# Kernel tuning notes

Hardware: AMD Instinct MI355X
Metric: run time of the kernel (lower is better)

## Reference

```python
import jax, jax.numpy as jnp
import numpy as np

L = 11
THETA_DIV = 5
OMEGA0 = 6
BLUR_K = 7
BLUR_SIGMA = 4.0


def _make_psi(j_scale):
    # Morlet wavelet bank exactly as np.fromfunction in the torch module
    c = L // 2
    k = np.arange(THETA_DIV, dtype=np.float64)[:, None, None]
    i = np.arange(L, dtype=np.float64)[None, :, None]
    jj = np.arange(L, dtype=np.float64)[None, None, :]
    scale = 2.0 * 2.0 ** (2 * j_scale)
    arg = (1j * OMEGA0 * ((i - c) * np.cos(np.pi * k / THETA_DIV)
                          - (jj - c) * np.sin(np.pi * k / THETA_DIV)) / scale
           - ((i - c) ** 2 + (jj - c) ** 2) / scale)
    return (1.0 / (np.sqrt(2.0 * np.pi) * 2.0 ** j_scale)) * np.exp(arg)


def _make_blur_kernel():
    # 7x7 Gaussian, sigma=4, normalized to sum 1 (standard GaussianBlur)
    c = (BLUR_K - 1) / 2.0
    x = np.arange(BLUR_K, dtype=np.float64) - c
    g = np.exp(-(x ** 2) / (2.0 * BLUR_SIGMA ** 2))
    k2 = np.outer(g, g)
    return (k2 / k2.sum()).astype(np.float32)


def setup_inputs() -> dict:
    key = jax.random.key(0)
    img = jax.random.normal(key, (8, 1, 256, 256), dtype=jnp.float32)
    psi = np.concatenate([_make_psi(3), _make_psi(0)], axis=0)  # [10,11,11] complex
    psi_re = jnp.asarray(psi.real.astype(np.float32)[:, None, :, :])  # [10,1,11,11]
    psi_im = jnp.asarray(psi.imag.astype(np.float32)[:, None, :, :])
    blur_k = jnp.asarray(_make_blur_kernel())  # [7,7]
    return {"img": img, "psi_re": psi_re, "psi_im": psi_im, "blur_k": blur_k}


def _conv(x, w, groups=1, pad=5):
    return jax.lax.conv_general_dilated(
        x, w, window_strides=(1, 1), padding=[(pad, pad), (pad, pad)],
        dimension_numbers=("NCHW", "OIHW", "NCHW"), feature_group_count=groups)


def _blur(x, blur_k):
    # depthwise Gaussian blur, padding 'same'
    C = x.shape[1]
    w = jnp.tile(blur_k[None, None], (C, 1, 1, 1))  # [C,1,7,7]
    return _conv(x, w, groups=C, pad=BLUR_K // 2)


def reference(img, psi_re, psi_im, blur_k):
    # s0: blurred input, strided downsample by 8
    s0 = _blur(img, blur_k)[:, :, ::8, ::8]

    # s1 = conv2d(img_complex, psi1): img is real, so split into re/im real convs
    s1_re = _conv(img, psi_re)            # [N,10,H,W]
    s1_im = _conv(img, psi_im)
    s1_abs = jnp.sqrt(s1_re * s1_re + s1_im * s1_im)
    # blurred s1 is later cast to double -> only its real part survives;
    # blur is a real-linear op so Re(blur(s1)) = blur(Re(s1))
    s1_out = _blur(s1_re, blur_k)[:, :, ::8, ::8]

    # s2 = grouped conv of |s1| with psi2 (psi1 tiled over 10 groups)
    psi2_re = jnp.tile(psi_re, (10, 1, 1, 1))  # [100,1,11,11]
    # only real part of blur(s2) reaches the output (cast to double)
    s2_re = _conv(s1_abs, psi2_re, groups=10)  # [N,100,H,W]
    s2_out = _blur(s2_re, blur_k)[:, :, ::8, ::8]

    feature = jnp.concatenate([s0, s1_out, s2_out], axis=1)  # [N,111,H/8,W/8]
    N = feature.shape[0]
    return feature.reshape(N, -1)
```

## Files before the change

### kernel.cpp

```cpp
#include <hip/hip_runtime.h>
#include <math.h>


#define PIMG_SZ (288 * 288)
#define FHP_OFF (8 * PIMG_SZ)
#define SSTR  284
#define W1    298
#define S1SZ  (17 * 298)
#define IVSTR 300
#define IVPL  (17 * 300)
#define CSTR  600

__global__ __launch_bounds__(256) void k_prep(const float* __restrict__ img,
                                              const float* __restrict__ psi_re,
                                              const float* __restrict__ psi_im,
                                              const float* __restrict__ blur,
                                              float* __restrict__ pimg,
                                              float* __restrict__ fhp) {
    int bid = blockIdx.x, tid = threadIdx.x;
    if (bid < 288) {
        int n = bid / 36, rg = bid - n * 36;
        float* dst = pimg + n * PIMG_SZ + rg * 8 * 288;
        const float* src = img + n * 65536;
        for (int i = tid; i < 576; i += 256) {
            int lr = i / 72, c4 = i - lr * 72;
            int prow = rg * 8 + lr;
            int irow = prow - 16;
            float4 v = {0.f, 0.f, 0.f, 0.f};
            if (irow >= 0 && irow < 256 && c4 >= 4 && c4 < 68)
                v = *(const float4*)(src + irow * 256 + 4 * c4 - 16);
            *(float4*)(dst + lr * 288 + 4 * c4) = v;
        }
        return;
    }
    for (int g = tid; g < 1360; g += 256) {
        int ch = g / 136;
        int w = g - ch * 136;
        int part = w / 17;
        int i = w - part * 17;
        const float* pr = psi_re + ch * 121;
        const float* pi = psi_im + ch * 121;
        float val = 0.f;
        if (part < 4) {
            int qmin = (part >= 2) ? 3 : 0;
            int comp = part & 1;
            float bden = blur[24];
            for (int q = qmin; q < 7; ++q) {
                int jj = i - q;
                if (jj < 0 || jj > 10) continue;
                float bq = blur[21 + q] / bden;
                float hh = comp ? pi[55 + jj] : pr[55 + jj];
                val += bq * hh;
            }
        } else {
            int pmin = (part >= 6) ? 3 : 0;
            int comp = part & 1;
            float dr = pr[60], di = pi[60];
            float inv = 1.f / (dr * dr + di * di);
            for (int p = pmin; p < 7; ++p) {
                int ii = i - p;
                if (ii < 0 || ii > 10) continue;
                float ap = blur[p * 7 + 3];
                float nr = pr[ii * 11 + 5], ni = pi[ii * 11 + 5];
                float f = comp ? (ni * dr - nr * di) * inv
                               : (nr * dr + ni * di) * inv;
                val += ap * f;
            }
        }
        fhp[g] = val;
    }
}

__global__ __launch_bounds__(512, 4) void k_fused4(const float* __restrict__ pimg,
                                                   const float* __restrict__ psi_re,
                                                   const float* __restrict__ psi_im,
                                                   const float* __restrict__ blur,
                                                   const float* __restrict__ fhp,
                                                   float* __restrict__ out) {
    __shared__ __align__(16) float bufA[10132];
    __shared__ __align__(16) float bufB[10200];
    const int tid = threadIdx.x;
    const int lane = tid & 63;
    const int wave = tid >> 6;
    const int Y = blockIdx.x;
    const int src2 = blockIdx.y;
    const int n = blockIdx.z;
    size_t nb = (size_t)n * 111 * 1024;

    const bool isimg = (src2 == 0);
    const bool paired = (src2 >= 3);
    int ga = 0, gb = 0;
    if (src2 == 1) ga = gb = 0;
    else if (src2 == 2) ga = gb = 5;
    else if (paired) {
        int p2 = src2 - 3;
        ga = (p2 < 2) ? 1 + p2 : 4 + p2;
        gb = (p2 < 2) ? 4 - p2 : 11 - p2;
    }

    if (isimg) {
        const float* gp = pimg + n * PIMG_SZ + (8 * Y + 8) * 288 + 8;
        for (int idx = tid; idx < 17 * 68; idx += 512) {
            int r = idx / 68, c4 = idx - r * 68;
            float4 v = *(const float4*)(gp + r * 288 + 4 * c4);
            int c = 4 * c4;
            int d = r * W1 + c + (c >> 3);
            bufA[d] = v.x; bufA[d + 1] = v.y; bufA[d + 2] = v.z; bufA[d + 3] = v.w;
        }
    } else {
        const float* pr = psi_re + ga * 121;
        const float* pi = psi_im + ga * 121;
        float dr = pr[60], di = pi[60];
        float inv = rsqrtf(dr * dr + di * di);

        const float* gp = pimg + n * PIMG_SZ + (8 * Y + 3) * 288 + 8;
        for (int idx = tid; idx < 27 * 68; idx += 512) {
            int r = idx / 68, c4 = idx - r * 68;
            *(float4*)(bufA + r * SSTR + 4 * c4) = *(const float4*)(gp + r * 288 + 4 * c4);
        }
        __syncthreads();

        for (int task = tid; task < 532; task += 512) {
            int rg = (task >= 266) ? 1 : 0;
            int v = task - rg * 266;
            int r0 = rg * 8;
            const float* sp = bufA + r0 * SSTR + v + 3;
            float xv[18];
#pragma unroll
            for (int p = 0; p < 18; ++p) xv[p] = sp[p * SSTR];
            int dsw = v + (v >> 3);
            float* dR = bufB + r0 * IVSTR + dsw;
#pragma unroll
            for (int m = 0; m < 8; ++m) {
                float ar = 0.f, ai = 0.f;
#pragma unroll
                for (int p = 0; p < 11; ++p) {
                    ar = fmaf(pr[p * 11 + 5], xv[m + p], ar);
                    ai = fmaf(pi[p * 11 + 5], xv[m + p], ai);
                }
                dR[m * IVSTR] = ar;
                dR[m * IVSTR + IVPL] = ai;
            }
        }
        if (tid < 266) {
            int v = tid;
            const float* sp = bufA + 16 * SSTR + v + 3;
            float ar = 0.f, ai = 0.f;
#pragma unroll
            for (int p = 0; p < 11; ++p) {
                float x = sp[p * SSTR];
                ar = fmaf(pr[p * 11 + 5], x, ar);
                ai = fmaf(pi[p * 11 + 5], x, ai);
            }
            int dsw = v + (v >> 3);
            bufB[16 * IVSTR + dsw] = ar;
            bufB[16 * IVSTR + IVPL + dsw] = ai;
        }
        __syncthreads();

        int rowbase = 8 * Y - 8;
        for (int t2 = tid; t2 < 544; t2 += 512) {
            int r = t2 >> 5, xg = t2 & 31;
            int ry = rowbase + r;
            int wb = r * W1 + 9 * xg + 9;
            if (ry >= 0 && ry < 256) {
                const float* sR = bufB + r * IVSTR + 9 * xg;
                float xr[18], xi[18];
#pragma unroll
                for (int j = 0; j < 18; ++j) {
                    int off = j + (j >> 3);
                    xr[j] = sR[off];
                    xi[j] = sR[off + IVPL];
                }
                if (paired) {
#pragma unroll
                    for (int m = 0; m < 8; ++m) {
                        float a = 0.f, b = 0.f, c = 0.f, d = 0.f;
#pragma unroll
                        for (int j = 0; j < 11; ++j) {
                            float hr = pr[55 + j], hi2 = pi[55 + j];
                            a = fmaf(hr, xr[m + j], a);
                            b = fmaf(hi2, xi[m + j], b);
                            c = fmaf(hr, xi[m + j], c);
                            d = fmaf(hi2, xr[m + j], d);
                        }
                        float e1 = a - b, o1 = c + d;
                        float e2 = a + b, o2 = c - d;
                        bufA[wb + m]        = inv * sqrtf(fmaf(e1, e1, o1 * o1));
                        bufA[S1SZ + wb + m] = inv * sqrtf(fmaf(e2, e2, o2 * o2));
                    }
                } else {
#pragma unroll
                    for (int m = 0; m < 8; ++m) {
                        float sr = 0.f, si = 0.f;
#pragma unroll
                        for (int j = 0; j < 11; ++j) {
                            float hr = pr[55 + j], hi2 = pi[55 + j];
                            sr = fmaf(hr, xr[m + j], fmaf(-hi2, xi[m + j], sr));
                            si = fmaf(hr, xi[m + j], fmaf(hi2, xr[m + j], si));
                        }
                        bufA[wb + m] = inv * sqrtf(fmaf(sr, sr, si * si));
                    }
                }
            } else {
#pragma unroll
                for (int m = 0; m < 8; ++m) {
                    bufA[wb + m] = 0.f;
                    if (paired) bufA[S1SZ + wb + m] = 0.f;
                }
            }
        }
        if (tid < 17) {
            int r = tid;
#pragma unroll
            for (int t = 0; t < 8; ++t) {
                bufA[r * W1 + t] = 0.f;
                if (paired) bufA[S1SZ + r * W1 + t] = 0.f;
            }
            bufA[r * W1 + 297] = 0.f;
            if (paired) bufA[S1SZ + r * W1 + 297] = 0.f;
        }
    }
    __syncthreads();

    {
        int kh = __builtin_amdgcn_readfirstlane(wave >> 2);
        int wl = wave & 3;
        int fro = (Y == 0) ? 102 : 68;
        int fio = (Y == 0) ? 119 : 85;
        const float* s1base = bufA + (paired ? kh * S1SZ : 0);
        int nk = paired ? 6 : 3;

        {
            int t = (wl << 6) + lane;
            int tsw = t + (t >> 3);
            float v[17];
#pragma unroll
            for (int i = 0; i < 17; ++i) v[i] = s1base[i * W1 + tsw];
            for (int kk = 0; kk < nk; ++kk) {
                int k, p;
                if (paired) { k = (kk < 3) ? kk : kk + 2; p = kh * 6 + kk; }
                else        { k = kh * 5 + kk;            p = kh * 3 + kk; }
                const float* fR = fhp + k * 136 + fro;
                const float* fI = fhp + k * 136 + fio;
                float cr = 0.f, ci = 0.f;
#pragma unroll
                for (int i = 0; i < 17; ++i) {
                    cr = fmaf(fR[i], v[i], cr);
                    ci = fmaf(fI[i], v[i], ci);
                }
                bufB[p * CSTR + tsw] = cr;
                bufB[p * CSTR + 300 + tsw] = ci;
            }
        }
        if (lane < 9) {
            int t = 256 + lane;
            int tsw = t + (t >> 3);
            float v[17];
#pragma unroll
            for (int i = 0; i < 17; ++i) v[i] = s1base[i * W1 + tsw];
            for (int kk = wl; kk < nk; kk += 4) {
                int k, p;
                if (paired) { k = (kk < 3) ? kk : kk + 2; p = kh * 6 + kk; }
                else        { k = kh * 5 + kk;            p = kh * 3 + kk; }
                const float* fR = fhp + k * 136 + fro;
                const float* fI = fhp + k * 136 + fio;
                float cr = 0.f, ci = 0.f;
#pragma unroll
                for (int i = 0; i < 17; ++i) {
                    cr = fmaf(fR[i], v[i], cr);
                    ci = fmaf(fI[i], v[i], ci);
                }
                bufB[p * CSTR + tsw] = cr;
                bufB[p * CSTR + 300 + tsw] = ci;
            }
        }
    }
    __syncthreads();

    int nout = paired ? 384 : 192;
    if (tid < nout) {
        int chsel = paired ? (tid >= 192) : 0;
        int t3 = tid - chsel * 192;
        int s = t3 >> 5, X = t3 & 31;
        int kdist = (s < 3) ? s : s + 2;
        int p = chsel * 6 + s;
        const float* hb = fhp + kdist * 136 + ((X == 0) ? 34 : 0);
        const float* cR = bufB + p * CSTR + 9 * X;
        float u = 0.f, v2 = 0.f;
#pragma unroll
        for (int j = 0; j < 17; ++j) {
            int off = j + (j >> 3);
            u  = fmaf(hb[j], cR[off], u);
            v2 = fmaf(hb[17 + j], cR[off + 300], v2);
        }
        int g = chsel ? gb : ga;
        int ch0 = isimg ? 1 : 11 + g * 10;
        out[nb + (size_t)(ch0 + kdist) * 1024 + Y * 32 + X] = u - v2;
        if (s == 1 || s == 2 || s == 4 || s == 5) {
            int partner = (s < 3) ? 5 - s : 13 - s;
            out[nb + (size_t)(ch0 + partner) * 1024 + Y * 32 + X] = u + v2;
        }
    } else if (isimg && tid < 224) {
        int X = tid - 192;
        float s0 = 0.f;
#pragma unroll
        for (int p = 0; p < 7; ++p)
#pragma unroll
            for (int q = 0; q < 7; ++q) {
                int c = 8 * X + q + 5;
                s0 = fmaf(blur[p * 7 + q], bufA[(p + 5) * W1 + c + (c >> 3)], s0);
            }
        out[nb + Y * 32 + X] = s0;
    }
}

extern "C" void kernel_launch(void* const* d_in, const int* in_sizes, int n_in,
                              void* d_out, int out_size, void* d_ws, size_t ws_size,
                              hipStream_t stream) {
    const float* img    = (const float*)d_in[0];
    const float* psi_re = (const float*)d_in[1];
    const float* psi_im = (const float*)d_in[2];
    const float* blur   = (const float*)d_in[3];
    float* out = (float*)d_out;
    float* ws = (float*)d_ws;
    float* pimg = ws;
    float* fhp  = ws + FHP_OFF;

    k_prep<<<289, 256, 0, stream>>>(img, psi_re, psi_im, blur, pimg, fhp);

    dim3 g2(32, 7, 8);
    k_fused4<<<g2, 512, 0, stream>>>(pimg, psi_re, psi_im, blur, fhp, out);
}
```

Baseline: 59.74 us.

## Pack intermediates as bf16 pairs in shared memory and serialize paired sources

Stores the vertical-pass intermediate (re/im) and the |s1| planes as packed bf16 pairs in LDS, roughly halving shared-memory footprint. The paired-source blur stage is restructured to process the two sources one after another through a single bufB region, with an extra barrier between them. The smaller LDS allows raising launch bounds from 4 to 6 blocks per CU for more occupancy. In exchange it loses precision (bf16 rounding of intermediates, including the raw image for s0) and serializes the paired work.

Result: no change. 58.78 us (-1.6%).

```diff
diff --git a/kernel.cpp b/kernel.cpp
--- a/kernel.cpp
+++ b/kernel.cpp
@@ -4,12 +4,20 @@
 
 #define PIMG_SZ (288 * 288)
 #define FHP_OFF (8 * PIMG_SZ)
-#define SSTR  284
+#define SSTR  276
 #define W1    298
-#define S1SZ  (17 * 298)
 #define IVSTR 300
-#define IVPL  (17 * 300)
 #define CSTR  600
+
+static __device__ __forceinline__ unsigned packbf2(float a, float b) {
+    unsigned ua = __float_as_uint(a);
+    unsigned ub = __float_as_uint(b);
+    ua = (ua + 0x7FFFu + ((ua >> 16) & 1u)) >> 16;
+    ub = (ub + 0x7FFFu + ((ub >> 16) & 1u)) & 0xFFFF0000u;
+    return ua | ub;
+}
+static __device__ __forceinline__ float unplo(unsigned u) { return __uint_as_float(u << 16); }
+static __device__ __forceinline__ float unphi(unsigned u) { return __uint_as_float(u & 0xFFFF0000u); }
 
 __global__ __launch_bounds__(256) void k_prep(const float* __restrict__ img,
                                               const float* __restrict__ psi_re,
@@ -71,14 +79,16 @@
     }
 }
 
-__global__ __launch_bounds__(512, 4) void k_fused4(const float* __restrict__ pimg,
+__global__ __launch_bounds__(512, 6) void k_fused5(const float* __restrict__ pimg,
                                                    const float* __restrict__ psi_re,
                                                    const float* __restrict__ psi_im,
                                                    const float* __restrict__ blur,
                                                    const float* __restrict__ fhp,
                                                    float* __restrict__ out) {
-    __shared__ __align__(16) float bufA[10132];
-    __shared__ __align__(16) float bufB[10200];
+    __shared__ __align__(16) float bufA[7452];
+    __shared__ __align__(16) float bufB[5100];
+    unsigned* s1P = (unsigned*)bufA;
+    unsigned* ivP = (unsigned*)bufB;
     const int tid = threadIdx.x;
     const int lane = tid & 63;
     const int wave = tid >> 6;
@@ -105,7 +115,12 @@
             float4 v = *(const float4*)(gp + r * 288 + 4 * c4);
             int c = 4 * c4;
             int d = r * W1 + c + (c >> 3);
-            bufA[d] = v.x; bufA[d + 1] = v.y; bufA[d + 2] = v.z; bufA[d + 3] = v.w;
+            float vs[4] = {v.x, v.y, v.z, v.w};
+#pragma unroll
+            for (int e = 0; e < 4; ++e) {
+                float val = (c + e > 264) ? 0.f : vs[e];
+                s1P[d + e] = packbf2(val, val);
+            }
         }
     } else {
         const float* pr = psi_re + ga * 121;
@@ -129,7 +144,7 @@
 #pragma unroll
             for (int p = 0; p < 18; ++p) xv[p] = sp[p * SSTR];
             int dsw = v + (v >> 3);
-            float* dR = bufB + r0 * IVSTR + dsw;
+            unsigned* dP = ivP + r0 * IVSTR + dsw;
 #pragma unroll
             for (int m = 0; m < 8; ++m) {
                 float ar = 0.f, ai = 0.f;
@@ -138,8 +153,7 @@
                     ar = fmaf(pr[p * 11 + 5], xv[m + p], ar);
                     ai = fmaf(pi[p * 11 + 5], xv[m + p], ai);
                 }
-                dR[m * IVSTR] = ar;
-                dR[m * IVSTR + IVPL] = ai;
+                dP[m * IVSTR] = packbf2(ar, ai);
             }
         }
         if (tid < 266) {
@@ -152,9 +166,7 @@
                 ar = fmaf(pr[p * 11 + 5], x, ar);
                 ai = fmaf(pi[p * 11 + 5], x, ai);
             }
-            int dsw = v + (v >> 3);
-            bufB[16 * IVSTR + dsw] = ar;
-            bufB[16 * IVSTR + IVPL + dsw] = ai;
+            ivP[16 * IVSTR + v + (v >> 3)] = packbf2(ar, ai);
         }
         __syncthreads();
 
@@ -164,13 +176,13 @@
             int ry = rowbase + r;
             int wb = r * W1 + 9 * xg + 9;
             if (ry >= 0 && ry < 256) {
-                const float* sR = bufB + r * IVSTR + 9 * xg;
+                const unsigned* sP = ivP + r * IVSTR + 9 * xg;
                 float xr[18], xi[18];
 #pragma unroll
                 for (int j = 0; j < 18; ++j) {
-                    int off = j + (j >> 3);
-                    xr[j] = sR[off];
-                    xi[j] = sR[off + IVPL];
+                    unsigned u = sP[j + (j >> 3)];
+                    xr[j] = unplo(u);
+                    xi[j] = unphi(u);
                 }
                 if (paired) {
 #pragma unroll
@@ -186,8 +198,8 @@
                         }
                         float e1 = a - b, o1 = c + d;
                         float e2 = a + b, o2 = c - d;
-                        bufA[wb + m]        = inv * sqrtf(fmaf(e1, e1, o1 * o1));
-                        bufA[S1SZ + wb + m] = inv * sqrtf(fmaf(e2, e2, o2 * o2));
+                        s1P[wb + m] = packbf2(inv * sqrtf(fmaf(e1, e1, o1 * o1)),
+                                              inv * sqrtf(fmaf(e2, e2, o2 * o2)));
                     }
                 } else {
 #pragma unroll
@@ -199,48 +211,66 @@
                             sr = fmaf(hr, xr[m + j], fmaf(-hi2, xi[m + j], sr));
                             si = fmaf(hr, xi[m + j], fmaf(hi2, xr[m + j], si));
                         }
-                        bufA[wb + m] = inv * sqrtf(fmaf(sr, sr, si * si));
+                        float val = inv * sqrtf(fmaf(sr, sr, si * si));
+                        s1P[wb + m] = packbf2(val, val);
                     }
                 }
             } else {
 #pragma unroll
-                for (int m = 0; m < 8; ++m) {
-                    bufA[wb + m] = 0.f;
-                    if (paired) bufA[S1SZ + wb + m] = 0.f;
-                }
+                for (int m = 0; m < 8; ++m) s1P[wb + m] = 0u;
             }
         }
         if (tid < 17) {
             int r = tid;
 #pragma unroll
-            for (int t = 0; t < 8; ++t) {
-                bufA[r * W1 + t] = 0.f;
-                if (paired) bufA[S1SZ + r * W1 + t] = 0.f;
-            }
-            bufA[r * W1 + 297] = 0.f;
-            if (paired) bufA[S1SZ + r * W1 + 297] = 0.f;
+            for (int t = 0; t < 8; ++t) s1P[r * W1 + t] = 0u;
+            s1P[r * W1 + 297] = 0u;
         }
     }
     __syncthreads();
 
-    {
-        int kh = __builtin_amdgcn_readfirstlane(wave >> 2);
-        int wl = wave & 3;
-        int fro = (Y == 0) ? 102 : 68;
-        int fio = (Y == 0) ? 119 : 85;
-        const float* s1base = bufA + (paired ? kh * S1SZ : 0);
-        int nk = paired ? 6 : 3;
-
+    const int nsrc = paired ? 2 : 1;
+    for (int sh = 0; sh < nsrc; ++sh) {
         {
-            int t = (wl << 6) + lane;
-            int tsw = t + (t >> 3);
-            float v[17];
-#pragma unroll
-            for (int i = 0; i < 17; ++i) v[i] = s1base[i * W1 + tsw];
-            for (int kk = 0; kk < nk; ++kk) {
-                int k, p;
-                if (paired) { k = (kk < 3) ? kk : kk + 2; p = kh * 6 + kk; }
-                else        { k = kh * 5 + kk;            p = kh * 3 + kk; }
+            int kh = __builtin_amdgcn_readfirstlane(wave >> 2);
+            int wl = wave & 3;
+            int fro = (Y == 0) ? 102 : 68;
+            int fio = (Y == 0) ? 119 : 85;
+            {
+                int t = (wl << 6) + lane;
+                int tsw = t + (t >> 3);
+                float v[17];
+#pragma unroll
+                for (int i = 0; i < 17; ++i) {
+                    unsigned u = s1P[i * W1 + tsw];
+                    v[i] = sh ? unphi(u) : unplo(u);
+                }
+                for (int kk = 0; kk < 3; ++kk) {
+                    int k = kh * 5 + kk;
+                    int p = kh * 3 + kk;
+                    const float* fR = fhp + k * 136 + fro;
+                    const float* fI = fhp + k * 136 + fio;
+                    float cr = 0.f, ci = 0.f;
+#pragma unroll
+                    for (int i = 0; i < 17; ++i) {
+                        cr = fmaf(fR[i], v[i], cr);
+                        ci = fmaf(fI[i], v[i], ci);
+                    }
+                    bufB[p * CSTR + tsw] = cr;
+                    bufB[p * CSTR + 300 + tsw] = ci;
+                }
+            }
+            int wv = __builtin_amdgcn_readfirstlane(wave);
+            if (wv < 6 && lane < 9) {
+                int t = 256 + lane;
+                int tsw = t + (t >> 3);
+                float v[17];
+#pragma unroll
+                for (int i = 0; i < 17; ++i) {
+                    unsigned u = s1P[i * W1 + tsw];
+                    v[i] = sh ? unphi(u) : unplo(u);
+                }
+                int k = (wv < 3) ? wv : wv + 2;
                 const float* fR = fhp + k * 136 + fro;
                 const float* fI = fhp + k * 136 + fio;
                 float cr = 0.f, ci = 0.f;
@@ -249,69 +279,45 @@
                     cr = fmaf(fR[i], v[i], cr);
                     ci = fmaf(fI[i], v[i], ci);
                 }
-                bufB[p * CSTR + tsw] = cr;
-                bufB[p * CSTR + 300 + tsw] = ci;
-            }
-        }
-        if (lane < 9) {
-            int t = 256 + lane;
-            int tsw = t + (t >> 3);
-            float v[17];
-#pragma unroll
-            for (int i = 0; i < 17; ++i) v[i] = s1base[i * W1 + tsw];
-            for (int kk = wl; kk < nk; kk += 4) {
-                int k, p;
-                if (paired) { k = (kk < 3) ? kk : kk + 2; p = kh * 6 + kk; }
-                else        { k = kh * 5 + kk;            p = kh * 3 + kk; }
-                const float* fR = fhp + k * 136 + fro;
-                const float* fI = fhp + k * 136 + fio;
-                float cr = 0.f, ci = 0.f;
-#pragma unroll
-                for (int i = 0; i < 17; ++i) {
-                    cr = fmaf(fR[i], v[i], cr);
-                    ci = fmaf(fI[i], v[i], ci);
-                }
-                bufB[p * CSTR + tsw] = cr;
-                bufB[p * CSTR + 300 + tsw] = ci;
-            }
-        }
-    }
-    __syncthreads();
-
-    int nout = paired ? 384 : 192;
-    if (tid < nout) {
-        int chsel = paired ? (tid >= 192) : 0;
-        int t3 = tid - chsel * 192;
-        int s = t3 >> 5, X = t3 & 31;
-        int kdist = (s < 3) ? s : s + 2;
-        int p = chsel * 6 + s;
-        const float* hb = fhp + kdist * 136 + ((X == 0) ? 34 : 0);
-        const float* cR = bufB + p * CSTR + 9 * X;
-        float u = 0.f, v2 = 0.f;
-#pragma unroll
-        for (int j = 0; j < 17; ++j) {
-            int off = j + (j >> 3);
-            u  = fmaf(hb[j], cR[off], u);
-            v2 = fmaf(hb[17 + j], cR[off + 300], v2);
-        }
-        int g = chsel ? gb : ga;
-        int ch0 = isimg ? 1 : 11 + g * 10;
-        out[nb + (size_t)(ch0 + kdist) * 1024 + Y * 32 + X] = u - v2;
-        if (s == 1 || s == 2 || s == 4 || s == 5) {
-            int partner = (s < 3) ? 5 - s : 13 - s;
-            out[nb + (size_t)(ch0 + partner) * 1024 + Y * 32 + X] = u + v2;
-        }
-    } else if (isimg && tid < 224) {
-        int X = tid - 192;
-        float s0 = 0.f;
-#pragma unroll
-        for (int p = 0; p < 7; ++p)
-#pragma unroll
-            for (int q = 0; q < 7; ++q) {
-                int c = 8 * X + q + 5;
-                s0 = fmaf(blur[p * 7 + q], bufA[(p + 5) * W1 + c + (c >> 3)], s0);
-            }
-        out[nb + Y * 32 + X] = s0;
+                bufB[wv * CSTR + tsw] = cr;
+                bufB[wv * CSTR + 300 + tsw] = ci;
+            }
+        }
+        __syncthreads();
+
+        if (tid < 192) {
+            int s = tid >> 5, X = tid & 31;
+            int kdist = (s < 3) ? s : s + 2;
+            const float* hb = fhp + kdist * 136 + ((X == 0) ? 34 : 0);
+            const float* cR = bufB + s * CSTR + 9 * X;
+            float u = 0.f, v2 = 0.f;
+#pragma unroll
+            for (int j = 0; j < 17; ++j) {
+                int off = j + (j >> 3);
+                u  = fmaf(hb[j], cR[off], u);
+                v2 = fmaf(hb[17 + j], cR[off + 300], v2);
+            }
+            int g = sh ? gb : ga;
+            int ch0 = isimg ? 1 : 11 + g * 10;
+            out[nb + (size_t)(ch0 + kdist) * 1024 + Y * 32 + X] = u - v2;
+            if (s == 1 || s == 2 || s == 4 || s == 5) {
+                int partner = (s < 3) ? 5 - s : 13 - s;
+                out[nb + (size_t)(ch0 + partner) * 1024 + Y * 32 + X] = u + v2;
+            }
+        } else if (isimg && tid < 224) {
+            int X = tid - 192;
+            float s0 = 0.f;
+#pragma unroll
+            for (int p = 0; p < 7; ++p)
+#pragma unroll
+                for (int q = 0; q < 7; ++q) {
+                    int c = 8 * X + q + 5;
+                    s0 = fmaf(blur[p * 7 + q],
+                              unplo(s1P[(p + 5) * W1 + c + (c >> 3)]), s0);
+                }
+            out[nb + Y * 32 + X] = s0;
+        }
+        if (sh + 1 < nsrc) __syncthreads();
     }
 }
 
@@ -330,5 +336,5 @@
     k_prep<<<289, 256, 0, stream>>>(img, psi_re, psi_im, blur, pimg, fhp);
 
     dim3 g2(32, 7, 8);
-    k_fused4<<<g2, 512, 0, stream>>>(pimg, psi_re, psi_im, blur, fhp, out);
+    k_fused5<<<g2, 512, 0, stream>>>(pimg, psi_re, psi_im, blur, fhp, out);
 }
```
